# Kernel optimization log

Hardware: AMD Instinct MI355X
Metric: run time of the kernel (lower is better)

## Reference

```python
import jax, jax.numpy as jnp
import numpy as np

B, SQ, SK = 2, 2048, 2048
D_MODEL, N_HEADS = 1024, 16
D_HEAD = D_MODEL // N_HEADS
LN_EPS = 1e-5


def _ln(x, w, b):
    # per-head LayerNorm over last dim (d_head)
    mu = jnp.mean(x, axis=-1, keepdims=True)
    var = jnp.mean(jnp.square(x - mu), axis=-1, keepdims=True)
    return (x - mu) * jax.lax.rsqrt(var + LN_EPS) * w + b


def setup_inputs() -> dict:
    key = jax.random.key(0)
    ks = jax.random.split(key, 8)
    sd = 1.0 / np.sqrt(D_MODEL)
    so = 1.0 / np.sqrt(D_HEAD)
    return {
        "x_q": jax.random.normal(ks[0], (B, SQ, D_MODEL), jnp.float32),
        "x_kv": jax.random.normal(ks[1], (B, SK, D_MODEL), jnp.float32),
        "mask": jnp.tril(jnp.ones((SQ, SK), dtype=bool)),  # causal
        "W_Q": jax.random.normal(ks[2], (N_HEADS, D_MODEL, D_HEAD), jnp.float32) * sd,
        "W_K": jax.random.normal(ks[3], (N_HEADS, D_MODEL, D_HEAD), jnp.float32) * sd,
        "W_V": jax.random.normal(ks[4], (N_HEADS, D_MODEL, D_HEAD), jnp.float32) * sd,
        "W_O": jax.random.normal(ks[5], (N_HEADS, D_HEAD, D_MODEL), jnp.float32) * so,
        "b_Q": jnp.zeros((N_HEADS, D_HEAD), jnp.float32),
        "b_K": jnp.zeros((N_HEADS, D_HEAD), jnp.float32),
        "b_V": jnp.zeros((N_HEADS, D_HEAD), jnp.float32),
        "b_O": jnp.zeros((D_MODEL,), jnp.float32),
        "ln1_w": jnp.ones((D_HEAD,), jnp.float32),
        "ln1_b": jnp.zeros((D_HEAD,), jnp.float32),
        "ln2_w": jnp.ones((D_HEAD,), jnp.float32),
        "ln2_b": jnp.zeros((D_HEAD,), jnp.float32),
    }


def reference(x_q, x_kv, mask, W_Q, W_K, W_V, W_O, b_Q, b_K, b_V, b_O,
              ln1_w, ln1_b, ln2_w, ln2_b):
    # QKV projections: b s d, n d h -> b s n h
    q = jnp.einsum('bsd,ndh->bsnh', x_q, W_Q) + b_Q
    k = jnp.einsum('bsd,ndh->bsnh', x_kv, W_K) + b_K
    v = jnp.einsum('bsd,ndh->bsnh', x_kv, W_V) + b_V
    # QK-norm (ln_first=False, rope=None -> just apply LN after projections)
    q = _ln(q, ln1_w, ln1_b)
    k = _ln(k, ln2_w, ln2_b)
    # NOTE: no 1/sqrt(d_head) scaling, matching the original module
    att = jnp.einsum('bqnh,bknh->bnqk', q, k)
    att = jnp.where(mask, att, -jnp.inf)
    probas = jax.nn.softmax(att, axis=-1)
    z = jnp.einsum('bnqk,bknh->bqnh', probas, v)
    out = jnp.einsum('bqnh,nhd->bqd', z, W_O) + b_O
    return (out, k, v)
```

## Files before the change

### kernel.cpp

```cpp
#include <hip/hip_runtime.h>
#include <hip/hip_bf16.h>

#define B_   2
#define SQ_  2048
#define DM_  1024
#define NH_  16
#define DH_  64

typedef __attribute__((ext_vector_type(8))) short          bf16x8;
typedef __attribute__((ext_vector_type(4))) short          bf16x4;
typedef __attribute__((ext_vector_type(8))) unsigned short u16x8;
typedef __attribute__((ext_vector_type(4))) float          f32x4;

__device__ __forceinline__ unsigned short f2bf(float f) {
    union { __hip_bfloat16 h; unsigned short u; } c;
    c.h = __float2bfloat16(f);
    return c.u;
}
__device__ __forceinline__ float gsum16(float v) {
    v += __shfl_xor(v, 1);
    v += __shfl_xor(v, 2);
    v += __shfl_xor(v, 4);
    v += __shfl_xor(v, 8);
    return v;
}

__device__ __forceinline__ f32x4 mfma16(bf16x4 a, bf16x4 b, f32x4 c) {
#if __has_builtin(__builtin_amdgcn_mfma_f32_16x16x16bf16_1k)
    return __builtin_amdgcn_mfma_f32_16x16x16bf16_1k(a, b, c, 0, 0, 0);
#else
    asm("v_mfma_f32_16x16x16_bf16 %0, %1, %2, %0" : "+v"(c) : "v"(a), "v"(b));
    return c;
#endif
}

__device__ __forceinline__ void gll16(const unsigned short* g, unsigned short* l) {
    __builtin_amdgcn_global_load_lds(
        (const __attribute__((address_space(1))) unsigned int*)g,
        (__attribute__((address_space(3))) unsigned int*)l,
        16, 0, 0);
}

__global__ __launch_bounds__(256) void prep_all(
    const float* __restrict__ W_Q, const float* __restrict__ W_K,
    const float* __restrict__ W_V, const float* __restrict__ W_O,
    const float* __restrict__ x_q, const float* __restrict__ x_kv,
    unsigned short* __restrict__ WTq, unsigned short* __restrict__ WTkv,
    unsigned short* __restrict__ WTo,
    unsigned short* __restrict__ xqbf, unsigned short* __restrict__ xkvbf)
{
    const int bid = blockIdx.x, tid = threadIdx.x;
    if (bid >= 1024) {
        const int cid = bid - 1024;
        const float* src = (cid < 512) ? x_q : x_kv;
        unsigned short* dst = (cid < 512) ? xqbf : xkvbf;
        const size_t base = (size_t)(cid & 511) * 8192 + tid * 4;
#pragma unroll
        for (int i = 0; i < 8; ++i) {
            const float4 v = *(const float4*)(src + base + i * 1024);
            ushort4 o;
            o.x = f2bf(v.x); o.y = f2bf(v.y); o.z = f2bf(v.z); o.w = f2bf(v.w);
            *(ushort4*)(dst + base + i * 1024) = o;
        }
        return;
    }
    __shared__ float t[64][65];
    const float* src; unsigned short* dst; int R, C, r0, c0;
    if (bid < 768) {
        const int which = bid >> 8, rem = bid & 255;
        const int rblk = rem & 15, zz = rem >> 4;
        src = (which == 0) ? W_Q : (which == 1) ? W_K : W_V;
        dst = (which == 0) ? WTq : (which == 1) ? WTkv : (WTkv + (1u << 20));
        src += (size_t)65536 * zz;
        dst += (size_t)65536 * zz;
        R = 1024; C = 64; r0 = rblk * 64; c0 = 0;
    } else {
        const int rem = bid - 768;
        src = W_O; dst = WTo; R = 1024; C = 1024;
        r0 = (rem & 15) * 64; c0 = (rem >> 4) * 64;
    }
    const int lr = tid >> 6, lc = tid & 63;
#pragma unroll
    for (int i = 0; i < 16; ++i)
        t[lr + i * 4][lc] = src[(size_t)(r0 + lr + i * 4) * C + c0 + lc];
    __syncthreads();
    const int u = tid & 15, w0 = tid >> 4;
#pragma unroll
    for (int i = 0; i < 4; ++i) {
        const int cl = w0 + i * 16;
        ushort4 o;
        o.x = f2bf(t[4 * u + 0][cl]);
        o.y = f2bf(t[4 * u + 1][cl]);
        o.z = f2bf(t[4 * u + 2][cl]);
        o.w = f2bf(t[4 * u + 3][cl]);
        *(ushort4*)&dst[(size_t)(c0 + cl) * R + r0 + 4 * u] = o;
    }
}

template <int TM, int MODE>
__device__ __forceinline__ void gemm_body(
    unsigned short (*__restrict__ As)[64], unsigned short (*__restrict__ Bs)[64],
    int bx, int by, const unsigned short* __restrict__ Abf,
    const unsigned short* __restrict__ WT,
    const float* __restrict__ biasK, const float* __restrict__ biasV,
    const float* __restrict__ lnw, const float* __restrict__ lnb,
    float* __restrict__ Cf, float* __restrict__ Cf2,
    unsigned short* __restrict__ Cb, unsigned short* __restrict__ CbT, int tid)
{
    constexpr int MI = (TM >= 32) ? TM / 32 : 1;
    constexpr int AJ = TM / 32;

    const int m0 = by * TM;
    const int c0 = bx * 128;

    const int wid = tid >> 6, lane = tid & 63;
    const int wm = (wid >> 1) * (TM / 2);
    const int wn = (wid & 1) * 64;
    const int l15 = lane & 15, qd = lane >> 4;

    const int srow  = tid >> 3;
    const int pslot = tid & 7;
    const int sslot = pslot ^ (srow & 7);
    const unsigned short* Ag = Abf + (size_t)(m0 + (srow % TM)) * 1024 + sslot * 8;
    const unsigned short* Bg = WT  + (size_t)(c0 + srow) * 1024 + sslot * 8;
    unsigned short* Al = &As[srow % TM][pslot * 8];
    unsigned short* Bl = &Bs[srow][pslot * 8];
    const bool athr = (srow < TM);

    const f32x4 zero4 = {0.f, 0.f, 0.f, 0.f};
    f32x4 acc[MI][4];
#pragma unroll
    for (int mi = 0; mi < MI; ++mi)
#pragma unroll
        for (int ni = 0; ni < 4; ++ni) acc[mi][ni] = zero4;

    const int r7 = l15 & 7;

    for (int kb = 0; kb < 16; ++kb) {
        const size_t kof = (size_t)kb * 64;
        __syncthreads();
        if (TM >= 64) {
#pragma unroll
            for (int j = 0; j < AJ; ++j)
                gll16(Ag + (size_t)j * 32 * 1024 + kof, Al + j * 32 * 64);
        } else if (athr) {
            gll16(Ag + kof, Al);
        }
#pragma unroll
        for (int j = 0; j < 4; ++j)
            gll16(Bg + (size_t)j * 32 * 1024 + kof, Bl + j * 32 * 64);
        __syncthreads();
#pragma unroll
        for (int ks = 0; ks < 2; ++ks) {
            const int cs = ((ks * 4 + qd) ^ r7) * 8;
            bf16x8 af[MI], bfr[4];
#pragma unroll
            for (int mi = 0; mi < MI; ++mi)
                af[mi] = *(const bf16x8*)&As[wm + mi * 16 + l15][cs];
#pragma unroll
            for (int ni = 0; ni < 4; ++ni)
                bfr[ni] = *(const bf16x8*)&Bs[wn + ni * 16 + l15][cs];
#pragma unroll
            for (int mi = 0; mi < MI; ++mi)
#pragma unroll
                for (int ni = 0; ni < 4; ++ni)
                    acc[mi][ni] = __builtin_amdgcn_mfma_f32_16x16x32_bf16(
                        af[mi], bfr[ni], acc[mi][ni], 0, 0, 0);
        }
    }

    const float* bias = (MODE == 1 && c0 >= 1024) ? biasV : biasK;
    float bv[4];
#pragma unroll
    for (int ni = 0; ni < 4; ++ni) bv[ni] = bias[(c0 + wn + ni * 16 + l15) & 1023];
#pragma unroll
    for (int mi = 0; mi < MI; ++mi)
#pragma unroll
        for (int ni = 0; ni < 4; ++ni)
#pragma unroll
            for (int r = 0; r < 4; ++r) acc[mi][ni][r] += bv[ni];

    if constexpr (MODE != 2) {
        const bool doLN = (MODE == 0) || (c0 < 1024);
        if (doLN) {
            float w4[4], lb4[4];
#pragma unroll
            for (int ni = 0; ni < 4; ++ni) {
                w4[ni]  = lnw[ni * 16 + l15];
                lb4[ni] = lnb[ni * 16 + l15];
            }
#pragma unroll
            for (int mi = 0; mi < MI; ++mi)
#pragma unroll
                for (int r = 0; r < 4; ++r) {
                    float s1 = acc[mi][0][r] + acc[mi][1][r] + acc[mi][2][r] + acc[mi][3][r];
                    const float mu = gsum16(s1) * (1.0f / 64.0f);
                    float s2 = acc[mi][0][r] * acc[mi][0][r] + acc[mi][1][r] * acc[mi][1][r]
                             + acc[mi][2][r] * acc[mi][2][r] + acc[mi][3][r] * acc[mi][3][r];
                    const float var = gsum16(s2) * (1.0f / 64.0f) - mu * mu;
                    const float rstd = rsqrtf(var + 1e-5f);
#pragma unroll
                    for (int ni = 0; ni < 4; ++ni)
                        acc[mi][ni][r] = (acc[mi][ni][r] - mu) * rstd * w4[ni] + lb4[ni];
                }
        }
    }

    if constexpr (MODE == 0) {
#pragma unroll
        for (int mi = 0; mi < MI; ++mi)
#pragma unroll
            for (int r = 0; r < 4; ++r) {
                const size_t grow = m0 + wm + mi * 16 + qd * 4 + r;
#pragma unroll
                for (int ni = 0; ni < 4; ++ni)
                    Cb[grow * 1024 + c0 + wn + ni * 16 + l15] = f2bf(acc[mi][ni][r]);
            }
    } else if constexpr (MODE == 2) {
#pragma unroll
        for (int mi = 0; mi < MI; ++mi)
#pragma unroll
            for (int r = 0; r < 4; ++r) {
                const size_t grow = m0 + wm + mi * 16 + qd * 4 + r;
#pragma unroll
                for (int ni = 0; ni < 4; ++ni)
                    Cf[grow * 1024 + c0 + wn + ni * 16 + l15] = acc[mi][ni][r];
            }
    } else {
        if (c0 < 1024) {
#pragma unroll
            for (int mi = 0; mi < MI; ++mi)
#pragma unroll
                for (int r = 0; r < 4; ++r) {
                    const size_t grow = m0 + wm + mi * 16 + qd * 4 + r;
#pragma unroll
                    for (int ni = 0; ni < 4; ++ni) {
                        const int gcol = c0 + wn + ni * 16 + l15;
                        Cf[grow * 1024 + gcol] = acc[mi][ni][r];
                        Cb[grow * 1024 + gcol] = f2bf(acc[mi][ni][r]);
                    }
                }
        } else {
#pragma unroll
            for (int mi = 0; mi < MI; ++mi) {
                const int growb = m0 + wm + mi * 16 + qd * 4;
                const int bb_ = growb >> 11, ss = growb & 2047;
#pragma unroll
                for (int ni = 0; ni < 4; ++ni) {
                    const int gv = c0 - 1024 + wn + ni * 16 + l15;
                    const int hh = gv >> 6, dd = gv & 63;
#pragma unroll
                    for (int r = 0; r < 4; ++r)
                        Cf2[(size_t)(growb + r) * 1024 + gv] = acc[mi][ni][r];
                    ushort4 w;
                    w.x = f2bf(acc[mi][ni][0]); w.y = f2bf(acc[mi][ni][1]);
                    w.z = f2bf(acc[mi][ni][2]); w.w = f2bf(acc[mi][ni][3]);
                    *(ushort4*)&CbT[(((size_t)bb_ * NH_ + hh) * DH_ + dd) * SQ_ + ss] = w;
                }
            }
        }
    }
}

__global__ __launch_bounds__(256) void qkv_fused(
    const unsigned short* __restrict__ xqbf, const unsigned short* __restrict__ xkvbf,
    const unsigned short* __restrict__ WTq, const unsigned short* __restrict__ WTkv,
    const float* __restrict__ b_Q, const float* __restrict__ b_K,
    const float* __restrict__ b_V,
    const float* __restrict__ ln1w, const float* __restrict__ ln1b,
    const float* __restrict__ ln2w, const float* __restrict__ ln2b,
    float* __restrict__ kout, float* __restrict__ vout,
    unsigned short* __restrict__ qz, unsigned short* __restrict__ kbf,
    unsigned short* __restrict__ vbfT)
{
    __shared__ __align__(16) unsigned short As[64][64];
    __shared__ __align__(16) unsigned short Bs[128][64];
    const int bid = blockIdx.x, tid = threadIdx.x;
    if (bid < 1024) {
        gemm_body<64, 1>(As, Bs, bid & 15, bid >> 4, xkvbf, WTkv, b_K, b_V,
                         ln2w, ln2b, kout, vout, kbf, vbfT, tid);
    } else {
        const int b2 = bid - 1024;
        gemm_body<64, 0>(As, Bs, b2 & 7, b2 >> 3, xqbf, WTq, b_Q, nullptr,
                         ln1w, ln1b, nullptr, nullptr, qz, nullptr, tid);
    }
}

__global__ __launch_bounds__(256) void o_gemm(
    const unsigned short* __restrict__ zbf, const unsigned short* __restrict__ WTo,
    const float* __restrict__ b_O, float* __restrict__ out)
{
    __shared__ __align__(16) unsigned short As[32][64];
    __shared__ __align__(16) unsigned short Bs[128][64];
    gemm_body<32, 2>(As, Bs, blockIdx.x, blockIdx.y, zbf, WTo, b_O, nullptr,
                     nullptr, nullptr, out, nullptr, nullptr, nullptr, threadIdx.x);
}

__global__ __launch_bounds__(256) void attn_mfma(
    unsigned short* __restrict__ qz, const unsigned short* __restrict__ kbf,
    const unsigned short* __restrict__ vbfT)
{
    __shared__ __align__(16) unsigned short Ks[2][64][72];
    __shared__ __align__(16) unsigned short VsT[2][64][72];

    const int tid = threadIdx.x;
    const int h = blockIdx.y, b = blockIdx.z;
    const int wid = tid >> 6, lane = tid & 63;
    const int l15 = lane & 15, qd = lane >> 4;
    const int srow = tid >> 2, scol = (tid & 3) * 16;

    const size_t kbase = (size_t)b * SQ_ * DM_ + (size_t)h * DH_;
    const size_t vbase = ((size_t)b * NH_ + h) * DH_ * (size_t)SQ_;
    const f32x4 zero4 = {0.f, 0.f, 0.f, 0.f};
    const float LOG2E = 1.44269504f, MBIAS = 46.1662413f;

    for (int pass = 0; pass < 2; ++pass) {
        const int qt = pass ? blockIdx.x : 31 - blockIdx.x;

        bf16x8 qf[2];
        {
            const unsigned short* qp =
                qz + kbase + (size_t)(qt * 64 + wid * 16 + l15) * DM_ + qd * 8;
            qf[0] = *(const bf16x8*)(qp);
            qf[1] = *(const bf16x8*)(qp + 32);
        }

        f32x4 z[4];
#pragma unroll
        for (int ni = 0; ni < 4; ++ni) z[ni] = zero4;
        float l_i = 0.f;

        {
            const unsigned short* ks = kbf + kbase + (size_t)srow * DM_ + scol;
            const u16x8 a0 = *(const u16x8*)(ks);
            const u16x8 a1 = *(const u16x8*)(ks + 8);
            const unsigned short* vs = vbfT + vbase + (size_t)srow * SQ_ + scol;
            const u16x8 b0 = *(const u16x8*)(vs);
            const u16x8 b1 = *(const u16x8*)(vs + 8);
            *(u16x8*)&Ks[0][srow][scol + 0]  = a0;
            *(u16x8*)&Ks[0][srow][scol + 8]  = a1;
            *(u16x8*)&VsT[0][srow][scol + 0] = b0;
            *(u16x8*)&VsT[0][srow][scol + 8] = b1;
        }
        __syncthreads();

        for (int kt = 0; kt <= qt; ++kt) {
            const int cur = kt & 1;

            u16x8 kr0, kr1, vr0, vr1;
            if (kt < qt) {
                const unsigned short* ks =
                    kbf + kbase + (size_t)((kt + 1) * 64 + srow) * DM_ + scol;
                kr0 = *(const u16x8*)(ks);
                kr1 = *(const u16x8*)(ks + 8);
                const unsigned short* vs =
                    vbfT + vbase + (size_t)srow * SQ_ + (kt + 1) * 64 + scol;
                vr0 = *(const u16x8*)(vs);
                vr1 = *(const u16x8*)(vs + 8);
            }

            f32x4 s[4];
#pragma unroll
            for (int mi = 0; mi < 4; ++mi) s[mi] = zero4;
#pragma unroll
            for (int ks2 = 0; ks2 < 2; ++ks2)
#pragma unroll
                for (int mi = 0; mi < 4; ++mi) {
                    const bf16x8 af =
                        *(const bf16x8*)&Ks[cur][mi * 16 + l15][ks2 * 32 + qd * 8];
                    s[mi] = __builtin_amdgcn_mfma_f32_16x16x32_bf16(af, qf[ks2], s[mi], 0, 0, 0);
                }

            if (kt == qt) {
#pragma unroll
                for (int mi = 0; mi < 4; ++mi)
#pragma unroll
                    for (int r = 0; r < 4; ++r)
                        if (mi * 16 + qd * 4 + r > wid * 16 + l15) s[mi][r] = -3.0e38f;
            }

            float ts[4];
            bf16x4 pa[4];
#pragma unroll
            for (int mi = 0; mi < 4; ++mi) {
#pragma unroll
                for (int r = 0; r < 4; ++r)
                    s[mi][r] = __builtin_amdgcn_exp2f(fmaf(s[mi][r], LOG2E, -MBIAS));
                ts[mi] = (s[mi][0] + s[mi][1]) + (s[mi][2] + s[mi][3]);
                pa[mi][0] = (short)f2bf(s[mi][0]);
                pa[mi][1] = (short)f2bf(s[mi][1]);
                pa[mi][2] = (short)f2bf(s[mi][2]);
                pa[mi][3] = (short)f2bf(s[mi][3]);
            }
            float rs = (ts[0] + ts[1]) + (ts[2] + ts[3]);
            rs += __shfl_xor(rs, 16);
            rs += __shfl_xor(rs, 32);
            l_i += rs;

#pragma unroll
            for (int mi = 0; mi < 4; ++mi)
#pragma unroll
                for (int ni = 0; ni < 4; ++ni) {
                    const bf16x4 bv =
                        *(const bf16x4*)&VsT[cur][ni * 16 + l15][mi * 16 + qd * 4];
                    z[ni] = mfma16(pa[mi], bv, z[ni]);
                }

            if (kt < qt) {
                *(u16x8*)&Ks[cur ^ 1][srow][scol + 0]  = kr0;
                *(u16x8*)&Ks[cur ^ 1][srow][scol + 8]  = kr1;
                *(u16x8*)&VsT[cur ^ 1][srow][scol + 0] = vr0;
                *(u16x8*)&VsT[cur ^ 1][srow][scol + 8] = vr1;
            }
            __syncthreads();
        }

        const float linv = 1.0f / l_i;
#pragma unroll
        for (int r = 0; r < 4; ++r) {
            const float lr_ = __shfl(linv, qd * 4 + r);
            const size_t row = (size_t)qt * 64 + wid * 16 + qd * 4 + r;
#pragma unroll
            for (int ni = 0; ni < 4; ++ni)
                qz[kbase + row * DM_ + ni * 16 + l15] = f2bf(z[ni][r] * lr_);
        }
    }
}

extern "C" void kernel_launch(void* const* d_in, const int* in_sizes, int n_in,
                              void* d_out, int out_size, void* d_ws, size_t ws_size,
                              hipStream_t stream)
{
    const float* x_q  = (const float*)d_in[0];
    const float* x_kv = (const float*)d_in[1];
    const float* W_Q  = (const float*)d_in[3];
    const float* W_K  = (const float*)d_in[4];
    const float* W_V  = (const float*)d_in[5];
    const float* W_O  = (const float*)d_in[6];
    const float* b_Q  = (const float*)d_in[7];
    const float* b_K  = (const float*)d_in[8];
    const float* b_V  = (const float*)d_in[9];
    const float* b_O  = (const float*)d_in[10];
    const float* ln1w = (const float*)d_in[11];
    const float* ln1b = (const float*)d_in[12];
    const float* ln2w = (const float*)d_in[13];
    const float* ln2b = (const float*)d_in[14];

    const size_t NTOK = (size_t)B_ * SQ_;
    float* out  = (float*)d_out;
    float* kout = out + NTOK * DM_;
    float* vout = kout + NTOK * DM_;

    unsigned short* xqbf  = (unsigned short*)out;
    unsigned short* xkvbf = xqbf + (1u << 22);

    unsigned short* wsu  = (unsigned short*)d_ws;
    unsigned short* WTq  = wsu;
    unsigned short* WTkv = WTq + (1u << 20);
    unsigned short* WTo  = WTkv + (2u << 20);
    unsigned short* qz   = WTo + (1u << 20);
    unsigned short* kbf  = qz + (1u << 22);
    unsigned short* vbfT = kbf + (1u << 22);

    prep_all<<<2048, 256, 0, stream>>>(W_Q, W_K, W_V, W_O, x_q, x_kv,
                                       WTq, WTkv, WTo, xqbf, xkvbf);

    qkv_fused<<<1536, 256, 0, stream>>>(xqbf, xkvbf, WTq, WTkv, b_Q, b_K, b_V,
                                        ln1w, ln1b, ln2w, ln2b,
                                        kout, vout, qz, kbf, vbfT);

    attn_mfma<<<dim3(16, NH_, B_), 256, 0, stream>>>(qz, kbf, vbfT);

    o_gemm<<<dim3(8, 128), 256, 0, stream>>>(qz, WTo, b_O, out);
}
```

Before: 233.1 us.

## Split attention KV tiles across two wave groups with shared-memory reduction

Doubles the attention block to 512 threads. Two groups of four waves each process alternating 64-key tiles from a 128-key staging buffer, then combine their partial outputs and row sums through shared memory. This replaces the old double buffer with a single buffer plus an extra barrier per step. The aim is to halve the serial KV loop length per block and raise wave-level parallelism, since the grid holds only 512 blocks. In exchange it adds a reduction step, idle waves on the odd final tile, and lower latency hiding from losing the double buffer.

```diff
diff --git a/kernel.cpp b/kernel.cpp
--- a/kernel.cpp
+++ b/kernel.cpp
@@ -296,31 +296,36 @@
                      nullptr, nullptr, out, nullptr, nullptr, nullptr, threadIdx.x);
 }
 
-__global__ __launch_bounds__(256) void attn_mfma(
+__global__ __launch_bounds__(512) void attn_mfma(
     unsigned short* __restrict__ qz, const unsigned short* __restrict__ kbf,
     const unsigned short* __restrict__ vbfT)
 {
-    __shared__ __align__(16) unsigned short Ks[2][64][72];
-    __shared__ __align__(16) unsigned short VsT[2][64][72];
+    __shared__ __align__(16) unsigned short Ks[128][72];
+    __shared__ __align__(16) unsigned short VsT[64][136];
 
     const int tid = threadIdx.x;
     const int h = blockIdx.y, b = blockIdx.z;
     const int wid = tid >> 6, lane = tid & 63;
+    const int g = wid & 3, p = wid >> 2;
     const int l15 = lane & 15, qd = lane >> 4;
     const int srow = tid >> 2, scol = (tid & 3) * 16;
+    const int vrow = tid >> 3, vcol = (tid & 7) * 16;
 
     const size_t kbase = (size_t)b * SQ_ * DM_ + (size_t)h * DH_;
     const size_t vbase = ((size_t)b * NH_ + h) * DH_ * (size_t)SQ_;
     const f32x4 zero4 = {0.f, 0.f, 0.f, 0.f};
     const float LOG2E = 1.44269504f, MBIAS = 46.1662413f;
 
+    float* zs = (float*)&Ks[0][0];
+    float* ls = (float*)&VsT[0][0];
+
     for (int pass = 0; pass < 2; ++pass) {
         const int qt = pass ? blockIdx.x : 31 - blockIdx.x;
 
         bf16x8 qf[2];
         {
             const unsigned short* qp =
-                qz + kbase + (size_t)(qt * 64 + wid * 16 + l15) * DM_ + qd * 8;
+                qz + kbase + (size_t)(qt * 64 + g * 16 + l15) * DM_ + qd * 8;
             qf[0] = *(const bf16x8*)(qp);
             qf[1] = *(const bf16x8*)(qp + 32);
         }
@@ -334,96 +339,118 @@
             const unsigned short* ks = kbf + kbase + (size_t)srow * DM_ + scol;
             const u16x8 a0 = *(const u16x8*)(ks);
             const u16x8 a1 = *(const u16x8*)(ks + 8);
-            const unsigned short* vs = vbfT + vbase + (size_t)srow * SQ_ + scol;
+            const unsigned short* vs = vbfT + vbase + (size_t)vrow * SQ_ + vcol;
             const u16x8 b0 = *(const u16x8*)(vs);
             const u16x8 b1 = *(const u16x8*)(vs + 8);
-            *(u16x8*)&Ks[0][srow][scol + 0]  = a0;
-            *(u16x8*)&Ks[0][srow][scol + 8]  = a1;
-            *(u16x8*)&VsT[0][srow][scol + 0] = b0;
-            *(u16x8*)&VsT[0][srow][scol + 8] = b1;
+            *(u16x8*)&Ks[srow][scol + 0]  = a0;
+            *(u16x8*)&Ks[srow][scol + 8]  = a1;
+            *(u16x8*)&VsT[vrow][vcol + 0] = b0;
+            *(u16x8*)&VsT[vrow][vcol + 8] = b1;
         }
         __syncthreads();
 
-        for (int kt = 0; kt <= qt; ++kt) {
-            const int cur = kt & 1;
-
+        const int NS = (qt >> 1) + 1;
+        for (int st = 0; st < NS; ++st) {
             u16x8 kr0, kr1, vr0, vr1;
-            if (kt < qt) {
+            if (st < NS - 1) {
                 const unsigned short* ks =
-                    kbf + kbase + (size_t)((kt + 1) * 64 + srow) * DM_ + scol;
+                    kbf + kbase + (size_t)((st + 1) * 128 + srow) * DM_ + scol;
                 kr0 = *(const u16x8*)(ks);
                 kr1 = *(const u16x8*)(ks + 8);
                 const unsigned short* vs =
-                    vbfT + vbase + (size_t)srow * SQ_ + (kt + 1) * 64 + scol;
+                    vbfT + vbase + (size_t)vrow * SQ_ + (st + 1) * 128 + vcol;
                 vr0 = *(const u16x8*)(vs);
                 vr1 = *(const u16x8*)(vs + 8);
             }
 
-            f32x4 s[4];
-#pragma unroll
-            for (int mi = 0; mi < 4; ++mi) s[mi] = zero4;
-#pragma unroll
-            for (int ks2 = 0; ks2 < 2; ++ks2)
+            const int kt = st * 2 + p;
+            if (kt <= qt) {
+                f32x4 s[4];
+#pragma unroll
+                for (int mi = 0; mi < 4; ++mi) s[mi] = zero4;
+#pragma unroll
+                for (int ks2 = 0; ks2 < 2; ++ks2)
+#pragma unroll
+                    for (int mi = 0; mi < 4; ++mi) {
+                        const bf16x8 af = *(const bf16x8*)
+                            &Ks[p * 64 + mi * 16 + l15][ks2 * 32 + qd * 8];
+                        s[mi] = __builtin_amdgcn_mfma_f32_16x16x32_bf16(
+                            af, qf[ks2], s[mi], 0, 0, 0);
+                    }
+
+                if (kt == qt) {
+#pragma unroll
+                    for (int mi = 0; mi < 4; ++mi)
+#pragma unroll
+                        for (int r = 0; r < 4; ++r)
+                            if (mi * 16 + qd * 4 + r > g * 16 + l15)
+                                s[mi][r] = -3.0e38f;
+                }
+
+                float ts[4];
+                bf16x4 pa[4];
 #pragma unroll
                 for (int mi = 0; mi < 4; ++mi) {
-                    const bf16x8 af =
-                        *(const bf16x8*)&Ks[cur][mi * 16 + l15][ks2 * 32 + qd * 8];
-                    s[mi] = __builtin_amdgcn_mfma_f32_16x16x32_bf16(af, qf[ks2], s[mi], 0, 0, 0);
+#pragma unroll
+                    for (int r = 0; r < 4; ++r)
+                        s[mi][r] = __builtin_amdgcn_exp2f(
+                            fmaf(s[mi][r], LOG2E, -MBIAS));
+                    ts[mi] = (s[mi][0] + s[mi][1]) + (s[mi][2] + s[mi][3]);
+                    pa[mi][0] = (short)f2bf(s[mi][0]);
+                    pa[mi][1] = (short)f2bf(s[mi][1]);
+                    pa[mi][2] = (short)f2bf(s[mi][2]);
+                    pa[mi][3] = (short)f2bf(s[mi][3]);
                 }
-
-            if (kt == qt) {
+                float rs = (ts[0] + ts[1]) + (ts[2] + ts[3]);
+                rs += __shfl_xor(rs, 16);
+                rs += __shfl_xor(rs, 32);
+                l_i += rs;
+
 #pragma unroll
                 for (int mi = 0; mi < 4; ++mi)
 #pragma unroll
-                    for (int r = 0; r < 4; ++r)
-                        if (mi * 16 + qd * 4 + r > wid * 16 + l15) s[mi][r] = -3.0e38f;
-            }
-
-            float ts[4];
-            bf16x4 pa[4];
-#pragma unroll
-            for (int mi = 0; mi < 4; ++mi) {
-#pragma unroll
-                for (int r = 0; r < 4; ++r)
-                    s[mi][r] = __builtin_amdgcn_exp2f(fmaf(s[mi][r], LOG2E, -MBIAS));
-                ts[mi] = (s[mi][0] + s[mi][1]) + (s[mi][2] + s[mi][3]);
-                pa[mi][0] = (short)f2bf(s[mi][0]);
-                pa[mi][1] = (short)f2bf(s[mi][1]);
-                pa[mi][2] = (short)f2bf(s[mi][2]);
-                pa[mi][3] = (short)f2bf(s[mi][3]);
-            }
-            float rs = (ts[0] + ts[1]) + (ts[2] + ts[3]);
-            rs += __shfl_xor(rs, 16);
-            rs += __shfl_xor(rs, 32);
-            l_i += rs;
-
-#pragma unroll
-            for (int mi = 0; mi < 4; ++mi)
-#pragma unroll
-                for (int ni = 0; ni < 4; ++ni) {
-                    const bf16x4 bv =
-                        *(const bf16x4*)&VsT[cur][ni * 16 + l15][mi * 16 + qd * 4];
-                    z[ni] = mfma16(pa[mi], bv, z[ni]);
-                }
-
-            if (kt < qt) {
-                *(u16x8*)&Ks[cur ^ 1][srow][scol + 0]  = kr0;
-                *(u16x8*)&Ks[cur ^ 1][srow][scol + 8]  = kr1;
-                *(u16x8*)&VsT[cur ^ 1][srow][scol + 0] = vr0;
-                *(u16x8*)&VsT[cur ^ 1][srow][scol + 8] = vr1;
+                    for (int ni = 0; ni < 4; ++ni) {
+                        const bf16x4 bv = *(const bf16x4*)
+                            &VsT[ni * 16 + l15][p * 64 + mi * 16 + qd * 4];
+                        z[ni] = mfma16(pa[mi], bv, z[ni]);
+                    }
             }
             __syncthreads();
-        }
-
-        const float linv = 1.0f / l_i;
-#pragma unroll
-        for (int r = 0; r < 4; ++r) {
-            const float lr_ = __shfl(linv, qd * 4 + r);
-            const size_t row = (size_t)qt * 64 + wid * 16 + qd * 4 + r;
+            if (st < NS - 1) {
+                *(u16x8*)&Ks[srow][scol + 0]  = kr0;
+                *(u16x8*)&Ks[srow][scol + 8]  = kr1;
+                *(u16x8*)&VsT[vrow][vcol + 0] = vr0;
+                *(u16x8*)&VsT[vrow][vcol + 8] = vr1;
+            }
+            __syncthreads();
+        }
+
+        if (p == 1) {
 #pragma unroll
             for (int ni = 0; ni < 4; ++ni)
-                qz[kbase + row * DM_ + ni * 16 + l15] = f2bf(z[ni][r] * lr_);
-        }
+                *(f32x4*)&zs[((g * 4 + ni) * 64 + lane) * 4] = z[ni];
+            ls[g * 64 + lane] = l_i;
+        }
+        __syncthreads();
+        if (p == 0) {
+            const float l_tot = l_i + ls[g * 64 + lane];
+#pragma unroll
+            for (int ni = 0; ni < 4; ++ni) {
+                const f32x4 zo = *(const f32x4*)&zs[((g * 4 + ni) * 64 + lane) * 4];
+#pragma unroll
+                for (int r = 0; r < 4; ++r) z[ni][r] += zo[r];
+            }
+            const float linv = 1.0f / l_tot;
+#pragma unroll
+            for (int r = 0; r < 4; ++r) {
+                const float lr_ = __shfl(linv, qd * 4 + r);
+                const size_t row = (size_t)qt * 64 + g * 16 + qd * 4 + r;
+#pragma unroll
+                for (int ni = 0; ni < 4; ++ni)
+                    qz[kbase + row * DM_ + ni * 16 + l15] = f2bf(z[ni][r] * lr_);
+            }
+        }
+        __syncthreads();
     }
 }
 
@@ -469,7 +496,7 @@
                                         ln1w, ln1b, ln2w, ln2b,
                                         kout, vout, qz, kbf, vbfT);
 
-    attn_mfma<<<dim3(16, NH_, B_), 256, 0, stream>>>(qz, kbf, vbfT);
+    attn_mfma<<<dim3(16, NH_, B_), 512, 0, stream>>>(qz, kbf, vbfT);
 
     o_gemm<<<dim3(8, 128), 256, 0, stream>>>(qz, WTo, b_O, out);
 }
```

After: 230.9 us. About the same (-0.9%).
